# Kernel optimization log

Hardware: AMD Instinct MI355X
Metric: run time of the kernel (lower is better)

## Reference

```python
import jax, jax.numpy as jnp
import numpy as np

N, E, S = 50000, 800000, 3          # nodes, edges, message-passing steps
ND, ED, GD = 7, 4, 2                # raw node/edge/global feature dims
H, L = 64, 64                       # hidden and latent sizes


def _mlp3(x, W0, b0, W1, b1, W2, b2):
    # MLP([H, H, L]) with gelu between layers, none after last (dropout off).
    x = jax.nn.gelu(x @ W0 + b0)
    x = jax.nn.gelu(x @ W1 + b1)
    return x @ W2 + b2


def _ln(x, scale, bias, eps=1e-6):
    mu = jnp.mean(x, axis=-1, keepdims=True)
    xc = x - mu
    var = jnp.mean(xc * xc, axis=-1, keepdims=True)
    return xc * jax.lax.rsqrt(var + eps) * scale + bias


def setup_inputs() -> dict:
    key = jax.random.key(0)
    ks = iter(jax.random.split(key, 40))

    def W(i, o, stacked=False):
        shape = (S, i, o) if stacked else (i, o)
        return (jax.random.normal(next(ks), shape, jnp.float32) / np.sqrt(i)).astype(jnp.float32)

    inp = {
        "nodes": jax.random.normal(next(ks), (N, ND), jnp.float32),
        "edges": jax.random.normal(next(ks), (E, ED), jnp.float32),
        "glob": jax.random.normal(next(ks), (1, GD), jnp.float32),
        # node embedder MLP [H,H,L]
        "emb_n_W0": W(ND, H), "emb_n_b0": jnp.zeros((H,), jnp.float32),
        "emb_n_W1": W(H, H), "emb_n_b1": jnp.zeros((H,), jnp.float32),
        "emb_n_W2": W(H, L), "emb_n_b2": jnp.zeros((L,), jnp.float32),
        # edge embedder MLP
        "emb_e_W0": W(ED, H), "emb_e_b0": jnp.zeros((H,), jnp.float32),
        "emb_e_W1": W(H, H), "emb_e_b1": jnp.zeros((H,), jnp.float32),
        "emb_e_W2": W(H, L), "emb_e_b2": jnp.zeros((L,), jnp.float32),
        # per-step edge update MLP: in = edges(L)+senders(L)+receivers(L)+glob(GD)
        "edge_W0": W(3 * L + GD, H, True), "edge_b0": jnp.zeros((S, H), jnp.float32),
        "edge_W1": W(H, H, True), "edge_b1": jnp.zeros((S, H), jnp.float32),
        "edge_W2": W(H, L, True), "edge_b2": jnp.zeros((S, L), jnp.float32),
        # per-step node update MLP: in = nodes(L)+received(L)+glob(GD)
        "node_W0": W(2 * L + GD, H, True), "node_b0": jnp.zeros((S, H), jnp.float32),
        "node_W1": W(H, H, True), "node_b1": jnp.zeros((S, H), jnp.float32),
        "node_W2": W(H, L, True), "node_b2": jnp.zeros((S, L), jnp.float32),
        # per-step LayerNorms for nodes and edges
        "ln_n_scale": jnp.ones((S, L), jnp.float32), "ln_n_bias": jnp.zeros((S, L), jnp.float32),
        "ln_e_scale": jnp.ones((S, L), jnp.float32), "ln_e_bias": jnp.zeros((S, L), jnp.float32),
        # decoder MLP [H,H,3]
        "dec_W0": W(L, H), "dec_b0": jnp.zeros((H,), jnp.float32),
        "dec_W1": W(H, H), "dec_b1": jnp.zeros((H,), jnp.float32),
        "dec_W2": W(H, 3), "dec_b2": jnp.zeros((3,), jnp.float32),
        "senders": jax.random.randint(next(ks), (E,), 0, N),
        "receivers": jax.random.randint(next(ks), (E,), 0, N),
    }
    return inp


def reference(nodes, edges, glob,
              emb_n_W0, emb_n_b0, emb_n_W1, emb_n_b1, emb_n_W2, emb_n_b2,
              emb_e_W0, emb_e_b0, emb_e_W1, emb_e_b1, emb_e_W2, emb_e_b2,
              edge_W0, edge_b0, edge_W1, edge_b1, edge_W2, edge_b2,
              node_W0, node_b0, node_W1, node_b1, node_W2, node_b2,
              ln_n_scale, ln_n_bias, ln_e_scale, ln_e_bias,
              dec_W0, dec_b0, dec_W1, dec_b1, dec_W2, dec_b2,
              senders, receivers):
    # GraphMapFeatures embedder
    n = _mlp3(nodes, emb_n_W0, emb_n_b0, emb_n_W1, emb_n_b1, emb_n_W2, emb_n_b2)  # [N, L]
    e = _mlp3(edges, emb_e_W0, emb_e_b0, emb_e_W1, emb_e_b1, emb_e_W2, emb_e_b2)  # [E, L]
    n_nodes, n_edges = n.shape[0], e.shape[0]
    ge = jnp.broadcast_to(glob, (n_edges, glob.shape[1]))  # globals per edge (single graph)
    gn = jnp.broadcast_to(glob, (n_nodes, glob.shape[1]))  # globals per node
    steps = edge_W0.shape[0]
    for s in range(steps):
        # edge update: gather sender/receiver node feats, concat, MLP
        e_in = jnp.concatenate([e, n[senders], n[receivers], ge], axis=1)  # [E, 3L+GD]
        new_e = _mlp3(e_in, edge_W0[s], edge_b0[s], edge_W1[s], edge_b1[s], edge_W2[s], edge_b2[s])
        # scatter-aggregate to receivers (jraph default: segment_sum)
        recv = jax.ops.segment_sum(new_e, receivers, num_segments=n_nodes)  # [N, L]
        n_in = jnp.concatenate([n, recv, gn], axis=1)  # [N, 2L+GD]
        new_n = _mlp3(n_in, node_W0[s], node_b0[s], node_W1[s], node_b1[s], node_W2[s], node_b2[s])
        # residual skip connections then per-step LayerNorm
        n = _ln(n + new_n, ln_n_scale[s], ln_n_bias[s])
        e = _ln(e + new_e, ln_e_scale[s], ln_e_bias[s])
    # decoder on nodes -> [N, 3]
    return _mlp3(n, dec_W0, dec_b0, dec_W1, dec_b1, dec_W2, dec_b2)
```

## Files before the change

### kernel.cpp

```cpp
#include <hip/hip_runtime.h>

#define N_NODES 50000
#define N_EDGES 800000
#define NSTEPS 3
#define NBLK_SCAN 196

typedef __attribute__((ext_vector_type(8))) short bf16x8;
typedef __attribute__((ext_vector_type(4))) float f32x4;


__device__ __forceinline__ float ldf(const void* p, long i, int bf) {
    if (bf) {
        unsigned int u = ((const unsigned short*)p)[i];
        u <<= 16;
        return __uint_as_float(u);
    }
    return ((const float*)p)[i];
}

__device__ __forceinline__ unsigned short f2bf(float f) {
    return (unsigned short)((__float_as_uint(f) + 0x8000u) >> 16);
}

__device__ __forceinline__ float bf2f(unsigned short u) {
    return __uint_as_float(((unsigned int)u) << 16);
}

__device__ __forceinline__ float gelu_f(float x) {
    float x2 = x * x;
    float m = x * fmaf(-0.10294325f, x2, -2.30220847f);
    float e = __builtin_amdgcn_exp2f(m);
    return x * __builtin_amdgcn_rcpf(1.0f + e);
}

__device__ __forceinline__ void zero4(f32x4 a[4]) {
#pragma unroll
    for (int t = 0; t < 4; t++) a[t] = (f32x4){0.f, 0.f, 0.f, 0.f};
}

__device__ __forceinline__ void mfma_chunk(f32x4 acc[4], bf16x8 a, const unsigned short* bb) {
    acc[0] = __builtin_amdgcn_mfma_f32_16x16x32_bf16(a, *(const bf16x8*)(bb + 0), acc[0], 0, 0, 0);
    acc[1] = __builtin_amdgcn_mfma_f32_16x16x32_bf16(a, *(const bf16x8*)(bb + 512), acc[1], 0, 0, 0);
    acc[2] = __builtin_amdgcn_mfma_f32_16x16x32_bf16(a, *(const bf16x8*)(bb + 1024), acc[2], 0, 0, 0);
    acc[3] = __builtin_amdgcn_mfma_f32_16x16x32_bf16(a, *(const bf16x8*)(bb + 1536), acc[3], 0, 0, 0);
}

__global__ void detect_kernel(const void* probe, int* flag) {
    if (threadIdx.x == 0 && blockIdx.x == 0) {
        unsigned int w = *(const unsigned int*)probe;
        *flag = (w == 0x3F803F80u) ? 1 : 0;
    }
}

__global__ void hist_kernel(const int* __restrict__ receivers, int* __restrict__ counts) {
    int i = blockIdx.x * 256 + threadIdx.x;
    if (i < N_EDGES) atomicAdd(&counts[receivers[i]], 1);
}

__global__ void scan_partial(const int* __restrict__ counts, int* __restrict__ base,
                             int* __restrict__ blockSums) {
    __shared__ int sm[256];
    int b = blockIdx.x, t = threadIdx.x, i = b * 256 + t;
    int v = (i < N_NODES) ? counts[i] : 0;
    sm[t] = v;
    __syncthreads();
    for (int off = 1; off < 256; off <<= 1) {
        int x = (t >= off) ? sm[t - off] : 0;
        __syncthreads();
        sm[t] += x;
        __syncthreads();
    }
    if (i < N_NODES) base[i] = sm[t] - v;
    if (t == 255) blockSums[b] = sm[255];
}

__global__ void scan_tops(int* __restrict__ blockSums, int* __restrict__ tops) {
    __shared__ int sm[256];
    int t = threadIdx.x;
    int v = (t < NBLK_SCAN) ? blockSums[t] : 0;
    sm[t] = v;
    __syncthreads();
    for (int off = 1; off < 256; off <<= 1) {
        int x = (t >= off) ? sm[t - off] : 0;
        __syncthreads();
        sm[t] += x;
        __syncthreads();
    }
    if (t < NBLK_SCAN) tops[t] = sm[t] - v;
}

__global__ void scan_add(int* __restrict__ base, const int* __restrict__ tops,
                         int* __restrict__ cursor) {
    int b = blockIdx.x, i = b * 256 + threadIdx.x;
    if (i < N_NODES) {
        int v = base[i] + tops[b];
        base[i] = v;
        cursor[i] = v;
    }
}

__global__ void scatter_kernel(const int* __restrict__ senders,
                               const int* __restrict__ receivers, int* __restrict__ cursor,
                               int* __restrict__ ss, int* __restrict__ rsrt,
                               int* __restrict__ perm) {
    int i = blockIdx.x * 256 + threadIdx.x;
    if (i < N_EDGES) {
        int r = receivers[i];
        int pos = atomicAdd(&cursor[r], 1);
        ss[pos] = senders[i];
        rsrt[pos] = r;
        perm[pos] = i;
    }
}

struct PrepPtrs {
    const void* W[14];
    const void* eb0;
    const void* nb0;
    const void* glob;
};

#define PREP_WTOTAL 139264
__global__ void prep_all(PrepPtrs p, unsigned short* WbBase, float* b0eff_e, float* b0eff_n,
                         const int* __restrict__ flagp) {
    const int totals[14] = {36864, 12288, 12288, 24576, 12288, 12288, 2048,
                            4096,  4096,  2048,  4096,  4096,  4096,  4096};
    const int ksrc[14] = {192, 64, 64, 128, 64, 64, 7, 64, 64, 4, 64, 64, 64, 64};
    const int sstride[14] = {12416, 4096, 4096, 8320, 4096, 4096, 448,
                             4096,  4096, 256,  4096, 4096, 4096, 4096};
    const int nch[14] = {6, 2, 2, 4, 2, 2, 1, 2, 2, 1, 2, 2, 2, 2};

    const int bf = *flagp;
    int i = blockIdx.x * 256 + threadIdx.x;
    if (i < PREP_WTOTAL) {
        int e = 0, base = 0;
        while (i >= base + totals[e]) { base += totals[e]; e++; }
        int il = i - base;
        int j = il & 7, lane = (il >> 3) & 63, t = (il >> 9) & 3;
        int c = (il >> 11) % nch[e], s = il / (2048 * nch[e]);
        int k = c * 32 + (lane >> 4) * 8 + j;
        int col = t * 16 + (lane & 15);
        WbBase[i] = (k < ksrc[e]) ? f2bf(ldf(p.W[e], (long)s * sstride[e] + (long)k * 64 + col, bf))
                                  : (unsigned short)0;
    } else if (i < PREP_WTOTAL + 384) {
        int i2 = i - PREP_WTOTAL;
        float g0 = ldf(p.glob, 0, bf), g1 = ldf(p.glob, 1, bf);
        if (i2 < 192) {
            int s = i2 >> 6, col = i2 & 63;
            b0eff_e[i2] = ldf(p.eb0, i2, bf) + g0 * ldf(p.W[0], (long)s * 12416 + 192 * 64 + col, bf)
                                             + g1 * ldf(p.W[0], (long)s * 12416 + 193 * 64 + col, bf);
        } else {
            int il = i2 - 192;
            int s = il >> 6, col = il & 63;
            b0eff_n[il] = ldf(p.nb0, il, bf) + g0 * ldf(p.W[3], (long)s * 8320 + 128 * 64 + col, bf)
                                             + g1 * ldf(p.W[3], (long)s * 8320 + 129 * 64 + col, bf);
        }
    }
}

template <int DIN, int OUT_BF>
__global__ __launch_bounds__(256) void embed_mfma(
    const void* __restrict__ xin, const unsigned short* __restrict__ Wb0, const void* b0,
    const unsigned short* __restrict__ Wb1, const void* b1,
    const unsigned short* __restrict__ Wb2, const void* b2, void* __restrict__ outp,
    unsigned short* __restrict__ out_bf, const int* __restrict__ perm, int R,
    const int* __restrict__ flagp) {
    __shared__ __align__(16) unsigned short Xs[64 * 40];
    __shared__ __align__(16) unsigned short hbuf[64 * 72];
    const int bf = *flagp;
    const int tid = threadIdx.x;
    const long rb = (long)blockIdx.x * 64;
    const int lane = tid & 63, w = tid >> 6, q = lane >> 4, l15 = lane & 15;
    const int arow = 16 * w + l15, aoff = q * 8;
    unsigned short* hw = hbuf + w * 16 * 72;

    {
        int r = tid >> 2, seg = tid & 3;
        long idx = rb + r;
        long src = (perm != nullptr && idx < R) ? (long)perm[idx] : idx;
        unsigned short u[8];
#pragma unroll
        for (int j = 0; j < 8; j++) {
            int col = seg * 8 + j;
            u[j] = (col < DIN && idx < R) ? f2bf(ldf(xin, src * DIN + col, bf)) : (unsigned short)0;
        }
        *(uint4*)&Xs[r * 40 + seg * 8] = *(uint4*)u;
    }

    f32x4 acc[4];
    zero4(acc);
    {
        bf16x8 a = *(const bf16x8*)&Xs[arow * 40 + aoff];
        mfma_chunk(acc, a, Wb0 + lane * 8);
#pragma unroll
        for (int t = 0; t < 4; t++) {
            int col = t * 16 + l15;
            float b = ldf(b0, col, bf);
#pragma unroll
            for (int reg = 0; reg < 4; reg++)
                hw[(q * 4 + reg) * 72 + col] = f2bf(gelu_f(acc[t][reg] + b));
        }
    }
    zero4(acc);
    {
#pragma unroll
        for (int c = 0; c < 2; c++) {
            bf16x8 a = *(const bf16x8*)&hw[l15 * 72 + c * 32 + aoff];
            mfma_chunk(acc, a, Wb1 + c * 2048 + lane * 8);
        }
#pragma unroll
        for (int t = 0; t < 4; t++) {
            int col = t * 16 + l15;
            float b = ldf(b1, col, bf);
#pragma unroll
            for (int reg = 0; reg < 4; reg++)
                hw[(q * 4 + reg) * 72 + col] = f2bf(gelu_f(acc[t][reg] + b));
        }
    }
    zero4(acc);
    {
#pragma unroll
        for (int c = 0; c < 2; c++) {
            bf16x8 a = *(const bf16x8*)&hw[l15 * 72 + c * 32 + aoff];
            mfma_chunk(acc, a, Wb2 + c * 2048 + lane * 8);
        }
    }
    if (OUT_BF) {
#pragma unroll
        for (int t = 0; t < 4; t++) {
            int col = t * 16 + l15;
            float b = ldf(b2, col, bf);
#pragma unroll
            for (int reg = 0; reg < 4; reg++)
                hw[(q * 4 + reg) * 72 + col] = f2bf(acc[t][reg] + b);
        }
#pragma unroll
        for (int p = 0; p < 2; p++) {
            int r = 16 * w + p * 8 + (lane >> 3), o = lane & 7;
            long idx = rb + r;
            if (idx < R)
                *(uint4*)&((unsigned short*)outp)[idx * 64 + o * 8] =
                    *(const uint4*)&hbuf[r * 72 + o * 8];
        }
    } else {
#pragma unroll
        for (int t = 0; t < 4; t++) {
            int col = t * 16 + l15;
            float b = ldf(b2, col, bf);
#pragma unroll
            for (int reg = 0; reg < 4; reg++) {
                long idx = rb + 16 * w + q * 4 + reg;
                if (idx < R) {
                    float v = acc[t][reg] + b;
                    ((float*)outp)[idx * 64 + col] = v;
                    out_bf[idx * 64 + col] = f2bf(v);
                }
            }
        }
    }
}

#define EST 72
#define NST 68
template <int S0, int LAST>
__global__ __launch_bounds__(256) void edge_step(
    unsigned short* __restrict__ e_lat, const unsigned short* __restrict__ n_bf,
    const int* __restrict__ ss, const int* __restrict__ rsrt, const int* __restrict__ perm,
    const void* __restrict__ xe_raw, const unsigned short* __restrict__ We0, const void* eb0_,
    const unsigned short* __restrict__ We1, const void* eb1_,
    const unsigned short* __restrict__ We2, const void* eb2_,
    const unsigned short* __restrict__ Wb0, const unsigned short* __restrict__ Wb1,
    const unsigned short* __restrict__ Wb2, const float* __restrict__ b0eff, const void* b1,
    const void* b2, const void* lnsc, const void* lnbi, float* __restrict__ recvbuf, int s,
    const int* __restrict__ flagp) {
    __shared__ __align__(16) unsigned short Ee[64 * EST];
    __shared__ __align__(16) unsigned short NsNr[128 * NST];
    __shared__ int rcvs[64];
    float* newe = (float*)NsNr;

    const int bf = *flagp;
    const int tid = threadIdx.x;
    const long rb = (long)blockIdx.x * 64;
    const int lane = tid & 63, w = tid >> 6, q = lane >> 4, l15 = lane & 15;
    const int arow = 16 * w + l15, aoff = q * 8;
    unsigned short* hw = Ee + w * 16 * EST;

#pragma unroll
    for (int p = 0; p < 2; p++) {
        int r = 16 * w + p * 8 + (lane >> 3), o = lane & 7;
        long node = ss[rb + r];
        *(uint4*)&NsNr[r * NST + o * 8] = ((const uint4*)(n_bf + node * 64))[o];
    }
#pragma unroll
    for (int p = 0; p < 2; p++) {
        int r = 16 * w + p * 8 + (lane >> 3), o = lane & 7;
        long node = rsrt[rb + r];
        *(uint4*)&NsNr[(64 + r) * NST + o * 8] = ((const uint4*)(n_bf + node * 64))[o];
    }
    if (lane < 16) rcvs[16 * w + lane] = rsrt[rb + 16 * w + lane];

    float ein[4][4];
    f32x4 acc[4];

    if (S0) {
        zero4(acc);
        {
            bf16x8 a = (bf16x8){0, 0, 0, 0, 0, 0, 0, 0};
            if (q == 0) {
                long src = perm[rb + arow];
                unsigned short u[8] = {0, 0, 0, 0, 0, 0, 0, 0};
#pragma unroll
                for (int j = 0; j < 4; j++) u[j] = f2bf(ldf(xe_raw, src * 4 + j, bf));
                a = *(const bf16x8*)u;
            }
            mfma_chunk(acc, a, We0 + lane * 8);
#pragma unroll
            for (int t = 0; t < 4; t++) {
                int col = t * 16 + l15;
                float b = ldf(eb0_, col, bf);
#pragma unroll
                for (int reg = 0; reg < 4; reg++)
                    hw[(q * 4 + reg) * EST + col] = f2bf(gelu_f(acc[t][reg] + b));
            }
        }
        zero4(acc);
        {
#pragma unroll
            for (int c = 0; c < 2; c++) {
                bf16x8 a = *(const bf16x8*)&hw[l15 * EST + c * 32 + aoff];
                mfma_chunk(acc, a, We1 + c * 2048 + lane * 8);
            }
#pragma unroll
            for (int t = 0; t < 4; t++) {
                int col = t * 16 + l15;
                float b = ldf(eb1_, col, bf);
#pragma unroll
                for (int reg = 0; reg < 4; reg++)
                    hw[(q * 4 + reg) * EST + col] = f2bf(gelu_f(acc[t][reg] + b));
            }
        }
        zero4(acc);
        {
#pragma unroll
            for (int c = 0; c < 2; c++) {
                bf16x8 a = *(const bf16x8*)&hw[l15 * EST + c * 32 + aoff];
                mfma_chunk(acc, a, We2 + c * 2048 + lane * 8);
            }
#pragma unroll
            for (int t = 0; t < 4; t++) {
                int col = t * 16 + l15;
                float b = ldf(eb2_, col, bf);
#pragma unroll
                for (int reg = 0; reg < 4; reg++) {
                    ein[reg][t] = acc[t][reg] + b;
                    Ee[(16 * w + q * 4 + reg) * EST + col] = f2bf(ein[reg][t]);
                }
            }
        }
    } else {
#pragma unroll
        for (int p = 0; p < 2; p++) {
            int r = 16 * w + p * 8 + (lane >> 3), o = lane & 7;
            *(uint4*)&Ee[r * EST + o * 8] = ((const uint4*)(e_lat + (rb + r) * 64))[o];
        }
        if (!LAST) {
#pragma unroll
            for (int reg = 0; reg < 4; reg++)
#pragma unroll
                for (int t = 0; t < 4; t++)
                    ein[reg][t] = bf2f(Ee[(16 * w + q * 4 + reg) * EST + t * 16 + l15]);
        }
    }

    zero4(acc);
    {
        const unsigned short* B = Wb0 + (long)s * 6 * 2048 + lane * 8;
#pragma unroll
        for (int c = 0; c < 2; c++) {
            bf16x8 a = *(const bf16x8*)&Ee[arow * EST + c * 32 + aoff];
            mfma_chunk(acc, a, B + c * 2048);
        }
#pragma unroll
        for (int c = 0; c < 2; c++) {
            bf16x8 a = *(const bf16x8*)&NsNr[arow * NST + c * 32 + aoff];
            mfma_chunk(acc, a, B + (2 + c) * 2048);
        }
#pragma unroll
        for (int c = 0; c < 2; c++) {
            bf16x8 a = *(const bf16x8*)&NsNr[(64 + arow) * NST + c * 32 + aoff];
            mfma_chunk(acc, a, B + (4 + c) * 2048);
        }
#pragma unroll
        for (int t = 0; t < 4; t++) {
            const int col = t * 16 + l15;
            const float b = b0eff[s * 64 + col];
#pragma unroll
            for (int reg = 0; reg < 4; reg++)
                hw[(q * 4 + reg) * EST + col] = f2bf(gelu_f(acc[t][reg] + b));
        }
    }
    zero4(acc);
    {
        const unsigned short* B = Wb1 + (long)s * 2 * 2048 + lane * 8;
#pragma unroll
        for (int c = 0; c < 2; c++) {
            bf16x8 a = *(const bf16x8*)&hw[l15 * EST + c * 32 + aoff];
            mfma_chunk(acc, a, B + c * 2048);
        }
#pragma unroll
        for (int t = 0; t < 4; t++) {
            const int col = t * 16 + l15;
            const float b = ldf(b1, (long)s * 64 + col, bf);
#pragma unroll
            for (int reg = 0; reg < 4; reg++)
                hw[(q * 4 + reg) * EST + col] = f2bf(gelu_f(acc[t][reg] + b));
        }
    }
    zero4(acc);
    {
        const unsigned short* B = Wb2 + (long)s * 2 * 2048 + lane * 8;
#pragma unroll
        for (int c = 0; c < 2; c++) {
            bf16x8 a = *(const bf16x8*)&hw[l15 * EST + c * 32 + aoff];
            mfma_chunk(acc, a, B + c * 2048);
        }
    }
    __syncthreads();

    float fin[4][4];
#pragma unroll
    for (int t = 0; t < 4; t++) {
        const float b = ldf(b2, (long)s * 64 + t * 16 + l15, bf);
#pragma unroll
        for (int reg = 0; reg < 4; reg++) fin[reg][t] = acc[t][reg] + b;
    }
    float lsc[4], lbi[4];
    if (!LAST) {
#pragma unroll
        for (int t = 0; t < 4; t++) {
            lsc[t] = ldf(lnsc, (long)s * 64 + t * 16 + l15, bf);
            lbi[t] = ldf(lnbi, (long)s * 64 + t * 16 + l15, bf);
        }
    }
#pragma unroll
    for (int reg = 0; reg < 4; reg++) {
        const int lr = q * 4 + reg;
#pragma unroll
        for (int t = 0; t < 4; t++) newe[w * 1056 + lr * 66 + t * 16 + l15] = fin[reg][t];
        if (!LAST) {
            float u[4], ssum = 0.f;
#pragma unroll
            for (int t = 0; t < 4; t++) {
                u[t] = ein[reg][t] + fin[reg][t];
                ssum += u[t];
            }
#pragma unroll
            for (int m = 1; m < 16; m <<= 1) ssum += __shfl_xor(ssum, m, 64);
            const float mu = ssum * (1.0f / 64.0f);
            float d[4], vv = 0.f;
#pragma unroll
            for (int t = 0; t < 4; t++) { d[t] = u[t] - mu; vv += d[t] * d[t]; }
#pragma unroll
            for (int m = 1; m < 16; m <<= 1) vv += __shfl_xor(vv, m, 64);
            const float rs = rsqrtf(vv * (1.0f / 64.0f) + 1e-6f);
#pragma unroll
            for (int t = 0; t < 4; t++)
                Ee[(16 * w + lr) * EST + t * 16 + l15] = f2bf(d[t] * rs * lsc[t] + lbi[t]);
        }
    }

    if (!LAST) {
#pragma unroll
        for (int p = 0; p < 2; p++) {
            int r = 16 * w + p * 8 + (lane >> 3), o = lane & 7;
            *(uint4*)&e_lat[(rb + r) * 64 + o * 8] = *(const uint4*)&Ee[r * EST + o * 8];
        }
    }
    {
        const int col = tid & 63, g = tid >> 6;
        float a = 0.f;
#pragma unroll
        for (int rr = 0; rr < 16; rr++) {
            const int r = 16 * g + rr;
            a += newe[g * 1056 + rr * 66 + col];
            if (rr == 15 || rcvs[r + 1] != rcvs[r]) {
                atomicAdd(&recvbuf[(long)rcvs[r] * 64 + col], a);
                a = 0.f;
            }
        }
    }
}

#define NXS 136
template <int FINAL>
__global__ __launch_bounds__(256) void node_update_mfma(
    float* __restrict__ n_lat, unsigned short* __restrict__ n_bf, float* __restrict__ recvbuf,
    const unsigned short* __restrict__ Wb0, const float* __restrict__ b0eff,
    const unsigned short* __restrict__ Wb1, const void* b1,
    const unsigned short* __restrict__ Wb2, const void* b2, const void* lnsc,
    const void* lnbi, const unsigned short* __restrict__ WbD0, const void* db0,
    const unsigned short* __restrict__ WbD1, const void* db1, const void* dW2,
    const void* db2, void* __restrict__ outp, int s, const int* __restrict__ flagp) {
    __shared__ __align__(16) unsigned short Xs[64 * NXS];
    __shared__ __align__(16) unsigned short hbuf[64 * 72];
    const int bf = *flagp;
    const int tid = threadIdx.x;
    const long rb = (long)blockIdx.x * 64;
    const int lane = tid & 63, w = tid >> 6, q = lane >> 4, l15 = lane & 15;
    const int arow = 16 * w + l15, aoff = q * 8;
    unsigned short* hw = hbuf + w * 16 * 72;

#pragma unroll
    for (int p = 0; p < 2; p++) {
        int r = 16 * w + p * 8 + (lane >> 3), o = lane & 7;
        long idx = rb + r;
        uint4 v = {0u, 0u, 0u, 0u};
        if (idx < N_NODES) v = ((const uint4*)(n_bf + idx * 64))[o];
        *(uint4*)&Xs[r * NXS + o * 8] = v;
    }
#pragma unroll
    for (int p = 0; p < 2; p++) {
        int r = 16 * w + p * 8 + (lane >> 3), o = lane & 7;
        long idx = rb + r;
        unsigned short u[8] = {0, 0, 0, 0, 0, 0, 0, 0};
        if (idx < N_NODES) {
            const float* src = recvbuf + idx * 64 + o * 8;
            float4 x0 = *(const float4*)src, x1 = *(const float4*)(src + 4);
            u[0] = f2bf(x0.x); u[1] = f2bf(x0.y); u[2] = f2bf(x0.z); u[3] = f2bf(x0.w);
            u[4] = f2bf(x1.x); u[5] = f2bf(x1.y); u[6] = f2bf(x1.z); u[7] = f2bf(x1.w);
        }
        *(uint4*)&Xs[r * NXS + 64 + o * 8] = *(uint4*)u;
    }

    f32x4 acc[4];
    zero4(acc);
    {
        const unsigned short* B = Wb0 + (long)s * 4 * 2048 + lane * 8;
#pragma unroll
        for (int c = 0; c < 4; c++) {
            bf16x8 a = *(const bf16x8*)&Xs[arow * NXS + c * 32 + aoff];
            mfma_chunk(acc, a, B + c * 2048);
        }
#pragma unroll
        for (int t = 0; t < 4; t++) {
            const int col = t * 16 + l15;
            const float b = b0eff[s * 64 + col];
#pragma unroll
            for (int reg = 0; reg < 4; reg++)
                hw[(q * 4 + reg) * 72 + col] = f2bf(gelu_f(acc[t][reg] + b));
        }
    }
    zero4(acc);
    {
        const unsigned short* B = Wb1 + (long)s * 2 * 2048 + lane * 8;
#pragma unroll
        for (int c = 0; c < 2; c++) {
            bf16x8 a = *(const bf16x8*)&hw[l15 * 72 + c * 32 + aoff];
            mfma_chunk(acc, a, B + c * 2048);
        }
#pragma unroll
        for (int t = 0; t < 4; t++) {
            const int col = t * 16 + l15;
            const float b = ldf(b1, (long)s * 64 + col, bf);
#pragma unroll
            for (int reg = 0; reg < 4; reg++)
                hw[(q * 4 + reg) * 72 + col] = f2bf(gelu_f(acc[t][reg] + b));
        }
    }
    zero4(acc);
    {
        const unsigned short* B = Wb2 + (long)s * 2 * 2048 + lane * 8;
#pragma unroll
        for (int c = 0; c < 2; c++) {
            bf16x8 a = *(const bf16x8*)&hw[l15 * 72 + c * 32 + aoff];
            mfma_chunk(acc, a, B + c * 2048);
        }
    }
    float b2v[4], lsc[4], lbi[4];
#pragma unroll
    for (int t = 0; t < 4; t++) {
        b2v[t] = ldf(b2, (long)s * 64 + t * 16 + l15, bf);
        lsc[t] = ldf(lnsc, (long)s * 64 + t * 16 + l15, bf);
        lbi[t] = ldf(lnbi, (long)s * 64 + t * 16 + l15, bf);
    }
#pragma unroll
    for (int reg = 0; reg < 4; reg++) {
        const int rowl = 16 * w + q * 4 + reg;
        const long idx = rb + rowl;
        const bool valid = idx < N_NODES;
        float u[4], ssum = 0.f;
#pragma unroll
        for (int t = 0; t < 4; t++) {
            const int col = t * 16 + l15;
            float xn = valid ? n_lat[idx * 64 + col] : 0.f;
            u[t] = xn + acc[t][reg] + b2v[t];
            ssum += u[t];
        }
#pragma unroll
        for (int m = 1; m < 16; m <<= 1) ssum += __shfl_xor(ssum, m, 64);
        const float mu = ssum * (1.0f / 64.0f);
        float d[4], vv = 0.f;
#pragma unroll
        for (int t = 0; t < 4; t++) { d[t] = u[t] - mu; vv += d[t] * d[t]; }
#pragma unroll
        for (int m = 1; m < 16; m <<= 1) vv += __shfl_xor(vv, m, 64);
        const float rs = rsqrtf(vv * (1.0f / 64.0f) + 1e-6f);
        if (FINAL) {
#pragma unroll
            for (int t = 0; t < 4; t++) {
                const int col = t * 16 + l15;
                hw[(q * 4 + reg) * 72 + col] = f2bf(d[t] * rs * lsc[t] + lbi[t]);
            }
        } else if (valid) {
#pragma unroll
            for (int t = 0; t < 4; t++) {
                const int col = t * 16 + l15;
                float v = d[t] * rs * lsc[t] + lbi[t];
                n_lat[idx * 64 + col] = v;
                n_bf[idx * 64 + col] = f2bf(v);
                recvbuf[idx * 64 + col] = 0.f;
            }
        }
    }
    if (FINAL) {
        zero4(acc);
        {
#pragma unroll
            for (int c = 0; c < 2; c++) {
                bf16x8 a = *(const bf16x8*)&hw[l15 * 72 + c * 32 + aoff];
                mfma_chunk(acc, a, WbD0 + c * 2048 + lane * 8);
            }
#pragma unroll
            for (int t = 0; t < 4; t++) {
                const int col = t * 16 + l15;
                const float b = ldf(db0, col, bf);
#pragma unroll
                for (int reg = 0; reg < 4; reg++)
                    hw[(q * 4 + reg) * 72 + col] = f2bf(gelu_f(acc[t][reg] + b));
            }
        }
        zero4(acc);
        {
#pragma unroll
            for (int c = 0; c < 2; c++) {
                bf16x8 a = *(const bf16x8*)&hw[l15 * 72 + c * 32 + aoff];
                mfma_chunk(acc, a, WbD1 + c * 2048 + lane * 8);
            }
#pragma unroll
            for (int t = 0; t < 4; t++) {
                const int col = t * 16 + l15;
                const float b = ldf(db1, col, bf);
#pragma unroll
                for (int reg = 0; reg < 4; reg++)
                    hw[(q * 4 + reg) * 72 + col] = f2bf(gelu_f(acc[t][reg] + b));
            }
        }
        const int col = tid & 63;
        const int r0 = w * 16;
        if (col < 3) {
            float a[16];
            const float b = ldf(db2, col, bf);
#pragma unroll
            for (int i = 0; i < 16; i++) a[i] = b;
            for (int k = 0; k < 64; k++) {
                float wv = ldf(dW2, (long)k * 3 + col, bf);
#pragma unroll
                for (int i = 0; i < 16; i++) a[i] = fmaf(bf2f(hw[i * 72 + k]), wv, a[i]);
            }
            for (int i = 0; i < 16; i++) {
                const long idx = rb + r0 + i;
                if (idx < N_NODES) {
                    if (bf)
                        ((unsigned short*)outp)[idx * 3 + col] = f2bf(a[i]);
                    else
                        ((float*)outp)[idx * 3 + col] = a[i];
                }
            }
        }
    }
}

extern "C" void kernel_launch(void* const* d_in, const int* in_sizes, int n_in, void* d_out,
                              int out_size, void* d_ws, size_t ws_size, hipStream_t stream) {
    const void* nodes = d_in[0];
    const void* edges = d_in[1];
    const void* glob = d_in[2];
    const void *enW0 = d_in[3], *enb0 = d_in[4], *enW1 = d_in[5], *enb1 = d_in[6],
               *enW2 = d_in[7], *enb2 = d_in[8];
    const void *eeW0 = d_in[9], *eeb0 = d_in[10], *eeW1 = d_in[11], *eeb1 = d_in[12],
               *eeW2 = d_in[13], *eeb2 = d_in[14];
    const void *eW0 = d_in[15], *eb0 = d_in[16], *eW1 = d_in[17], *eb1 = d_in[18],
               *eW2 = d_in[19], *eb2 = d_in[20];
    const void *nW0 = d_in[21], *nb0 = d_in[22], *nW1 = d_in[23], *nb1 = d_in[24],
               *nW2 = d_in[25], *nb2 = d_in[26];
    const void *lnns = d_in[27], *lnnb = d_in[28], *lnes = d_in[29], *lneb = d_in[30];
    const void *dW0 = d_in[31], *db0 = d_in[32], *dW1 = d_in[33], *db1 = d_in[34],
               *dW2 = d_in[35], *db2 = d_in[36];
    const int* senders = (const int*)d_in[37];
    const int* receivers = (const int*)d_in[38];

    float* n_lat = (float*)d_ws;
    float* recvb = n_lat + 3200000;
    float* b0eff_e = recvb + 3200000;
    float* b0eff_n = b0eff_e + 192;
    int* flag = (int*)(b0eff_n + 192);
    unsigned short* e_lat = (unsigned short*)(b0eff_n + 256);
    unsigned short* n_bf = e_lat + 51200000;
    unsigned short* WbBase = n_bf + 3200000;
    unsigned short* WbE0 = WbBase;
    unsigned short* WbE1 = WbBase + 36864;
    unsigned short* WbE2 = WbBase + 49152;
    unsigned short* WbN0 = WbBase + 61440;
    unsigned short* WbN1 = WbBase + 86016;
    unsigned short* WbN2 = WbBase + 98304;
    unsigned short* WbNE0 = WbBase + 110592;
    unsigned short* WbNE1 = WbBase + 112640;
    unsigned short* WbNE2 = WbBase + 116736;
    unsigned short* WbEE0 = WbBase + 120832;
    unsigned short* WbEE1 = WbBase + 122880;
    unsigned short* WbEE2 = WbBase + 126976;
    unsigned short* WbD0 = WbBase + 131072;
    unsigned short* WbD1 = WbBase + 135168;
    int* counts = (int*)(WbBase + 139264 + 64);
    int* sbase = counts + N_NODES;
    int* cursor = sbase + N_NODES;
    int* blockSums = cursor + N_NODES;
    int* tops = blockSums + 256;
    int* ss = tops + 256;
    int* rsrt = ss + N_EDGES;
    int* perm = rsrt + N_EDGES;

    detect_kernel<<<1, 64, 0, stream>>>(lnns, flag);

    PrepPtrs pp;
    pp.W[0] = eW0;  pp.W[1] = eW1;  pp.W[2] = eW2;
    pp.W[3] = nW0;  pp.W[4] = nW1;  pp.W[5] = nW2;
    pp.W[6] = enW0; pp.W[7] = enW1; pp.W[8] = enW2;
    pp.W[9] = eeW0; pp.W[10] = eeW1; pp.W[11] = eeW2;
    pp.W[12] = dW0; pp.W[13] = dW1;
    pp.eb0 = eb0; pp.nb0 = nb0; pp.glob = glob;
    prep_all<<<(PREP_WTOTAL + 384 + 255) / 256, 256, 0, stream>>>(pp, WbBase, b0eff_e, b0eff_n,
                                                                  flag);
    hipMemsetAsync(recvb, 0, (size_t)N_NODES * 64 * sizeof(float), stream);
    hipMemsetAsync(counts, 0, (size_t)N_NODES * sizeof(int), stream);

    hist_kernel<<<(N_EDGES + 255) / 256, 256, 0, stream>>>(receivers, counts);
    scan_partial<<<NBLK_SCAN, 256, 0, stream>>>(counts, sbase, blockSums);
    scan_tops<<<1, 256, 0, stream>>>(blockSums, tops);
    scan_add<<<NBLK_SCAN, 256, 0, stream>>>(sbase, tops, cursor);
    scatter_kernel<<<(N_EDGES + 255) / 256, 256, 0, stream>>>(senders, receivers, cursor, ss,
                                                              rsrt, perm);

    embed_mfma<7, 0><<<(N_NODES + 63) / 64, 256, 0, stream>>>(
        nodes, WbNE0, enb0, WbNE1, enb1, WbNE2, enb2, n_lat, n_bf, (const int*)nullptr,
        N_NODES, flag);

    edge_step<1, 0><<<N_EDGES / 64, 256, 0, stream>>>(
        e_lat, n_bf, ss, rsrt, perm, edges, WbEE0, eeb0, WbEE1, eeb1, WbEE2, eeb2,
        WbE0, WbE1, WbE2, b0eff_e, eb1, eb2, lnes, lneb, recvb, 0, flag);
    node_update_mfma<0><<<(N_NODES + 63) / 64, 256, 0, stream>>>(
        n_lat, n_bf, recvb, WbN0, b0eff_n, WbN1, nb1, WbN2, nb2, lnns, lnnb,
        nullptr, nullptr, nullptr, nullptr, nullptr, nullptr, nullptr, 0, flag);

    edge_step<0, 0><<<N_EDGES / 64, 256, 0, stream>>>(
        e_lat, n_bf, ss, rsrt, perm, edges, WbEE0, eeb0, WbEE1, eeb1, WbEE2, eeb2,
        WbE0, WbE1, WbE2, b0eff_e, eb1, eb2, lnes, lneb, recvb, 1, flag);
    node_update_mfma<0><<<(N_NODES + 63) / 64, 256, 0, stream>>>(
        n_lat, n_bf, recvb, WbN0, b0eff_n, WbN1, nb1, WbN2, nb2, lnns, lnnb,
        nullptr, nullptr, nullptr, nullptr, nullptr, nullptr, nullptr, 1, flag);

    edge_step<0, 1><<<N_EDGES / 64, 256, 0, stream>>>(
        e_lat, n_bf, ss, rsrt, perm, edges, WbEE0, eeb0, WbEE1, eeb1, WbEE2, eeb2,
        WbE0, WbE1, WbE2, b0eff_e, eb1, eb2, lnes, lneb, recvb, 2, flag);
    node_update_mfma<1><<<(N_NODES + 63) / 64, 256, 0, stream>>>(
        n_lat, n_bf, recvb, WbN0, b0eff_n, WbN1, nb1, WbN2, nb2, lnns, lnnb,
        WbD0, db0, WbD1, db1, dW2, db2, d_out, 2, flag);
}
```

Measured before the change: 751.2 us.

## Store hidden activations in permuted column order with packed bf16 LDS writes

Stores intermediate activations in shared memory with a permuted column order (col t*16+l15 placed at l15*4+t), so each lane writes its four columns as one 8-byte store. Conversion uses the packed v_cvt_pk_bf16_f32 instruction. The weight rows of every following layer, and the decoder's last scalar weights, are permuted in prep to match. This replaces many scalar 2-byte LDS stores and conversions with fewer wide ones. The risk is LDS bank conflicts from the new layout, and any weight whose rows are not permuted consistently will give wrong results.

Result: faster. 670.0 us (-10.8%).

```diff
diff --git a/kernel.cpp b/kernel.cpp
--- a/kernel.cpp
+++ b/kernel.cpp
@@ -24,6 +24,12 @@
 
 __device__ __forceinline__ float bf2f(unsigned short u) {
     return __uint_as_float(((unsigned int)u) << 16);
+}
+
+__device__ __forceinline__ unsigned int cvtpk(float a, float b) {
+    unsigned int r;
+    asm("v_cvt_pk_bf16_f32 %0, %1, %2" : "=v"(r) : "v"(a), "v"(b));
+    return r;
 }
 
 __device__ __forceinline__ float gelu_f(float x) {
@@ -129,6 +135,7 @@
     const int sstride[14] = {12416, 4096, 4096, 8320, 4096, 4096, 448,
                              4096,  4096, 256,  4096, 4096, 4096, 4096};
     const int nch[14] = {6, 2, 2, 4, 2, 2, 1, 2, 2, 1, 2, 2, 2, 2};
+    const int rowperm[14] = {0, 1, 1, 0, 1, 1, 0, 1, 1, 0, 1, 1, 1, 1};
 
     const int bf = *flagp;
     int i = blockIdx.x * 256 + threadIdx.x;
@@ -140,7 +147,9 @@
         int c = (il >> 11) % nch[e], s = il / (2048 * nch[e]);
         int k = c * 32 + (lane >> 4) * 8 + j;
         int col = t * 16 + (lane & 15);
-        WbBase[i] = (k < ksrc[e]) ? f2bf(ldf(p.W[e], (long)s * sstride[e] + (long)k * 64 + col, bf))
+        int ks = k;
+        if (rowperm[e] || (e == 0 && k < 64)) ks = ((k & 3) << 4) | (k >> 2);
+        WbBase[i] = (k < ksrc[e]) ? f2bf(ldf(p.W[e], (long)s * sstride[e] + (long)ks * 64 + col, bf))
                                   : (unsigned short)0;
     } else if (i < PREP_WTOTAL + 384) {
         int i2 = i - PREP_WTOTAL;
@@ -192,13 +201,15 @@
     {
         bf16x8 a = *(const bf16x8*)&Xs[arow * 40 + aoff];
         mfma_chunk(acc, a, Wb0 + lane * 8);
-#pragma unroll
-        for (int t = 0; t < 4; t++) {
-            int col = t * 16 + l15;
-            float b = ldf(b0, col, bf);
-#pragma unroll
-            for (int reg = 0; reg < 4; reg++)
-                hw[(q * 4 + reg) * 72 + col] = f2bf(gelu_f(acc[t][reg] + b));
+        float bb[4];
+#pragma unroll
+        for (int t = 0; t < 4; t++) bb[t] = ldf(b0, t * 16 + l15, bf);
+#pragma unroll
+        for (int reg = 0; reg < 4; reg++) {
+            uint2 v;
+            v.x = cvtpk(gelu_f(acc[0][reg] + bb[0]), gelu_f(acc[1][reg] + bb[1]));
+            v.y = cvtpk(gelu_f(acc[2][reg] + bb[2]), gelu_f(acc[3][reg] + bb[3]));
+            *(uint2*)&hw[(q * 4 + reg) * 72 + l15 * 4] = v;
         }
     }
     zero4(acc);
@@ -208,13 +219,15 @@
             bf16x8 a = *(const bf16x8*)&hw[l15 * 72 + c * 32 + aoff];
             mfma_chunk(acc, a, Wb1 + c * 2048 + lane * 8);
         }
-#pragma unroll
-        for (int t = 0; t < 4; t++) {
-            int col = t * 16 + l15;
-            float b = ldf(b1, col, bf);
-#pragma unroll
-            for (int reg = 0; reg < 4; reg++)
-                hw[(q * 4 + reg) * 72 + col] = f2bf(gelu_f(acc[t][reg] + b));
+        float bb[4];
+#pragma unroll
+        for (int t = 0; t < 4; t++) bb[t] = ldf(b1, t * 16 + l15, bf);
+#pragma unroll
+        for (int reg = 0; reg < 4; reg++) {
+            uint2 v;
+            v.x = cvtpk(gelu_f(acc[0][reg] + bb[0]), gelu_f(acc[1][reg] + bb[1]));
+            v.y = cvtpk(gelu_f(acc[2][reg] + bb[2]), gelu_f(acc[3][reg] + bb[3]));
+            *(uint2*)&hw[(q * 4 + reg) * 72 + l15 * 4] = v;
         }
     }
     zero4(acc);
@@ -314,13 +327,15 @@
                 a = *(const bf16x8*)u;
             }
             mfma_chunk(acc, a, We0 + lane * 8);
-#pragma unroll
-            for (int t = 0; t < 4; t++) {
-                int col = t * 16 + l15;
-                float b = ldf(eb0_, col, bf);
-#pragma unroll
-                for (int reg = 0; reg < 4; reg++)
-                    hw[(q * 4 + reg) * EST + col] = f2bf(gelu_f(acc[t][reg] + b));
+            float bb[4];
+#pragma unroll
+            for (int t = 0; t < 4; t++) bb[t] = ldf(eb0_, t * 16 + l15, bf);
+#pragma unroll
+            for (int reg = 0; reg < 4; reg++) {
+                uint2 v;
+                v.x = cvtpk(gelu_f(acc[0][reg] + bb[0]), gelu_f(acc[1][reg] + bb[1]));
+                v.y = cvtpk(gelu_f(acc[2][reg] + bb[2]), gelu_f(acc[3][reg] + bb[3]));
+                *(uint2*)&hw[(q * 4 + reg) * EST + l15 * 4] = v;
             }
         }
         zero4(acc);
@@ -330,13 +345,15 @@
                 bf16x8 a = *(const bf16x8*)&hw[l15 * EST + c * 32 + aoff];
                 mfma_chunk(acc, a, We1 + c * 2048 + lane * 8);
             }
-#pragma unroll
-            for (int t = 0; t < 4; t++) {
-                int col = t * 16 + l15;
-                float b = ldf(eb1_, col, bf);
-#pragma unroll
-                for (int reg = 0; reg < 4; reg++)
-                    hw[(q * 4 + reg) * EST + col] = f2bf(gelu_f(acc[t][reg] + b));
+            float bb[4];
+#pragma unroll
+            for (int t = 0; t < 4; t++) bb[t] = ldf(eb1_, t * 16 + l15, bf);
+#pragma unroll
+            for (int reg = 0; reg < 4; reg++) {
+                uint2 v;
+                v.x = cvtpk(gelu_f(acc[0][reg] + bb[0]), gelu_f(acc[1][reg] + bb[1]));
+                v.y = cvtpk(gelu_f(acc[2][reg] + bb[2]), gelu_f(acc[3][reg] + bb[3]));
+                *(uint2*)&hw[(q * 4 + reg) * EST + l15 * 4] = v;
             }
         }
         zero4(acc);
@@ -346,15 +363,18 @@
                 bf16x8 a = *(const bf16x8*)&hw[l15 * EST + c * 32 + aoff];
                 mfma_chunk(acc, a, We2 + c * 2048 + lane * 8);
             }
-#pragma unroll
-            for (int t = 0; t < 4; t++) {
-                int col = t * 16 + l15;
-                float b = ldf(eb2_, col, bf);
-#pragma unroll
-                for (int reg = 0; reg < 4; reg++) {
-                    ein[reg][t] = acc[t][reg] + b;
-                    Ee[(16 * w + q * 4 + reg) * EST + col] = f2bf(ein[reg][t]);
-                }
+            float bb[4];
+#pragma unroll
+            for (int t = 0; t < 4; t++) bb[t] = ldf(eb2_, t * 16 + l15, bf);
+#pragma unroll
+            for (int reg = 0; reg < 4; reg++) {
+                float e0 = acc[0][reg] + bb[0], e1 = acc[1][reg] + bb[1];
+                float e2 = acc[2][reg] + bb[2], e3 = acc[3][reg] + bb[3];
+                ein[reg][0] = e0; ein[reg][1] = e1; ein[reg][2] = e2; ein[reg][3] = e3;
+                uint2 v;
+                v.x = cvtpk(e0, e1);
+                v.y = cvtpk(e2, e3);
+                *(uint2*)&Ee[(16 * w + q * 4 + reg) * EST + l15 * 4] = v;
             }
         }
     } else {
@@ -365,10 +385,13 @@
         }
         if (!LAST) {
 #pragma unroll
-            for (int reg = 0; reg < 4; reg++)
-#pragma unroll
-                for (int t = 0; t < 4; t++)
-                    ein[reg][t] = bf2f(Ee[(16 * w + q * 4 + reg) * EST + t * 16 + l15]);
+            for (int reg = 0; reg < 4; reg++) {
+                uint2 pv = *(const uint2*)&Ee[(16 * w + q * 4 + reg) * EST + l15 * 4];
+                ein[reg][0] = __uint_as_float(pv.x << 16);
+                ein[reg][1] = __uint_as_float(pv.x & 0xffff0000u);
+                ein[reg][2] = __uint_as_float(pv.y << 16);
+                ein[reg][3] = __uint_as_float(pv.y & 0xffff0000u);
+            }
         }
     }
 
@@ -390,13 +413,15 @@
             bf16x8 a = *(const bf16x8*)&NsNr[(64 + arow) * NST + c * 32 + aoff];
             mfma_chunk(acc, a, B + (4 + c) * 2048);
         }
-#pragma unroll
-        for (int t = 0; t < 4; t++) {
-            const int col = t * 16 + l15;
-            const float b = b0eff[s * 64 + col];
-#pragma unroll
-            for (int reg = 0; reg < 4; reg++)
-                hw[(q * 4 + reg) * EST + col] = f2bf(gelu_f(acc[t][reg] + b));
+        float bb[4];
+#pragma unroll
+        for (int t = 0; t < 4; t++) bb[t] = b0eff[s * 64 + t * 16 + l15];
+#pragma unroll
+        for (int reg = 0; reg < 4; reg++) {
+            uint2 v;
+            v.x = cvtpk(gelu_f(acc[0][reg] + bb[0]), gelu_f(acc[1][reg] + bb[1]));
+            v.y = cvtpk(gelu_f(acc[2][reg] + bb[2]), gelu_f(acc[3][reg] + bb[3]));
+            *(uint2*)&hw[(q * 4 + reg) * EST + l15 * 4] = v;
         }
     }
     zero4(acc);
@@ -407,13 +432,15 @@
             bf16x8 a = *(const bf16x8*)&hw[l15 * EST + c * 32 + aoff];
             mfma_chunk(acc, a, B + c * 2048);
         }
-#pragma unroll
-        for (int t = 0; t < 4; t++) {
-            const int col = t * 16 + l15;
-            const float b = ldf(b1, (long)s * 64 + col, bf);
-#pragma unroll
-            for (int reg = 0; reg < 4; reg++)
-                hw[(q * 4 + reg) * EST + col] = f2bf(gelu_f(acc[t][reg] + b));
+        float bb[4];
+#pragma unroll
+        for (int t = 0; t < 4; t++) bb[t] = ldf(b1, (long)s * 64 + t * 16 + l15, bf);
+#pragma unroll
+        for (int reg = 0; reg < 4; reg++) {
+            uint2 v;
+            v.x = cvtpk(gelu_f(acc[0][reg] + bb[0]), gelu_f(acc[1][reg] + bb[1]));
+            v.y = cvtpk(gelu_f(acc[2][reg] + bb[2]), gelu_f(acc[3][reg] + bb[3]));
+            *(uint2*)&hw[(q * 4 + reg) * EST + l15 * 4] = v;
         }
     }
     zero4(acc);
@@ -463,9 +490,10 @@
 #pragma unroll
             for (int m = 1; m < 16; m <<= 1) vv += __shfl_xor(vv, m, 64);
             const float rs = rsqrtf(vv * (1.0f / 64.0f) + 1e-6f);
-#pragma unroll
-            for (int t = 0; t < 4; t++)
-                Ee[(16 * w + lr) * EST + t * 16 + l15] = f2bf(d[t] * rs * lsc[t] + lbi[t]);
+            uint2 v;
+            v.x = cvtpk(d[0] * rs * lsc[0] + lbi[0], d[1] * rs * lsc[1] + lbi[1]);
+            v.y = cvtpk(d[2] * rs * lsc[2] + lbi[2], d[3] * rs * lsc[3] + lbi[3]);
+            *(uint2*)&Ee[(16 * w + lr) * EST + l15 * 4] = v;
         }
     }
 
@@ -522,14 +550,16 @@
     for (int p = 0; p < 2; p++) {
         int r = 16 * w + p * 8 + (lane >> 3), o = lane & 7;
         long idx = rb + r;
-        unsigned short u[8] = {0, 0, 0, 0, 0, 0, 0, 0};
+        uint4 v = {0u, 0u, 0u, 0u};
         if (idx < N_NODES) {
             const float* src = recvbuf + idx * 64 + o * 8;
             float4 x0 = *(const float4*)src, x1 = *(const float4*)(src + 4);
-            u[0] = f2bf(x0.x); u[1] = f2bf(x0.y); u[2] = f2bf(x0.z); u[3] = f2bf(x0.w);
-            u[4] = f2bf(x1.x); u[5] = f2bf(x1.y); u[6] = f2bf(x1.z); u[7] = f2bf(x1.w);
-        }
-        *(uint4*)&Xs[r * NXS + 64 + o * 8] = *(uint4*)u;
+            v.x = cvtpk(x0.x, x0.y);
+            v.y = cvtpk(x0.z, x0.w);
+            v.z = cvtpk(x1.x, x1.y);
+            v.w = cvtpk(x1.z, x1.w);
+        }
+        *(uint4*)&Xs[r * NXS + 64 + o * 8] = v;
     }
 
     f32x4 acc[4];
@@ -541,13 +571,15 @@
             bf16x8 a = *(const bf16x8*)&Xs[arow * NXS + c * 32 + aoff];
             mfma_chunk(acc, a, B + c * 2048);
         }
-#pragma unroll
-        for (int t = 0; t < 4; t++) {
-            const int col = t * 16 + l15;
-            const float b = b0eff[s * 64 + col];
-#pragma unroll
-            for (int reg = 0; reg < 4; reg++)
-                hw[(q * 4 + reg) * 72 + col] = f2bf(gelu_f(acc[t][reg] + b));
+        float bb[4];
+#pragma unroll
+        for (int t = 0; t < 4; t++) bb[t] = b0eff[s * 64 + t * 16 + l15];
+#pragma unroll
+        for (int reg = 0; reg < 4; reg++) {
+            uint2 v;
+            v.x = cvtpk(gelu_f(acc[0][reg] + bb[0]), gelu_f(acc[1][reg] + bb[1]));
+            v.y = cvtpk(gelu_f(acc[2][reg] + bb[2]), gelu_f(acc[3][reg] + bb[3]));
+            *(uint2*)&hw[(q * 4 + reg) * 72 + l15 * 4] = v;
         }
     }
     zero4(acc);
@@ -558,13 +590,15 @@
             bf16x8 a = *(const bf16x8*)&hw[l15 * 72 + c * 32 + aoff];
             mfma_chunk(acc, a, B + c * 2048);
         }
-#pragma unroll
-        for (int t = 0; t < 4; t++) {
-            const int col = t * 16 + l15;
-            const float b = ldf(b1, (long)s * 64 + col, bf);
-#pragma unroll
-            for (int reg = 0; reg < 4; reg++)
-                hw[(q * 4 + reg) * 72 + col] = f2bf(gelu_f(acc[t][reg] + b));
+        float bb[4];
+#pragma unroll
+        for (int t = 0; t < 4; t++) bb[t] = ldf(b1, (long)s * 64 + t * 16 + l15, bf);
+#pragma unroll
+        for (int reg = 0; reg < 4; reg++) {
+            uint2 v;
+            v.x = cvtpk(gelu_f(acc[0][reg] + bb[0]), gelu_f(acc[1][reg] + bb[1]));
+            v.y = cvtpk(gelu_f(acc[2][reg] + bb[2]), gelu_f(acc[3][reg] + bb[3]));
+            *(uint2*)&hw[(q * 4 + reg) * 72 + l15 * 4] = v;
         }
     }
     zero4(acc);
@@ -606,11 +640,10 @@
         for (int m = 1; m < 16; m <<= 1) vv += __shfl_xor(vv, m, 64);
         const float rs = rsqrtf(vv * (1.0f / 64.0f) + 1e-6f);
         if (FINAL) {
-#pragma unroll
-            for (int t = 0; t < 4; t++) {
-                const int col = t * 16 + l15;
-                hw[(q * 4 + reg) * 72 + col] = f2bf(d[t] * rs * lsc[t] + lbi[t]);
-            }
+            uint2 v;
+            v.x = cvtpk(d[0] * rs * lsc[0] + lbi[0], d[1] * rs * lsc[1] + lbi[1]);
+            v.y = cvtpk(d[2] * rs * lsc[2] + lbi[2], d[3] * rs * lsc[3] + lbi[3]);
+            *(uint2*)&hw[(q * 4 + reg) * 72 + l15 * 4] = v;
         } else if (valid) {
 #pragma unroll
             for (int t = 0; t < 4; t++) {
@@ -630,13 +663,15 @@
                 bf16x8 a = *(const bf16x8*)&hw[l15 * 72 + c * 32 + aoff];
                 mfma_chunk(acc, a, WbD0 + c * 2048 + lane * 8);
             }
-#pragma unroll
-            for (int t = 0; t < 4; t++) {
-                const int col = t * 16 + l15;
-                const float b = ldf(db0, col, bf);
-#pragma unroll
-                for (int reg = 0; reg < 4; reg++)
-                    hw[(q * 4 + reg) * 72 + col] = f2bf(gelu_f(acc[t][reg] + b));
+            float bb[4];
+#pragma unroll
+            for (int t = 0; t < 4; t++) bb[t] = ldf(db0, t * 16 + l15, bf);
+#pragma unroll
+            for (int reg = 0; reg < 4; reg++) {
+                uint2 v;
+                v.x = cvtpk(gelu_f(acc[0][reg] + bb[0]), gelu_f(acc[1][reg] + bb[1]));
+                v.y = cvtpk(gelu_f(acc[2][reg] + bb[2]), gelu_f(acc[3][reg] + bb[3]));
+                *(uint2*)&hw[(q * 4 + reg) * 72 + l15 * 4] = v;
             }
         }
         zero4(acc);
@@ -646,13 +681,15 @@
                 bf16x8 a = *(const bf16x8*)&hw[l15 * 72 + c * 32 + aoff];
                 mfma_chunk(acc, a, WbD1 + c * 2048 + lane * 8);
             }
-#pragma unroll
-            for (int t = 0; t < 4; t++) {
-                const int col = t * 16 + l15;
-                const float b = ldf(db1, col, bf);
-#pragma unroll
-                for (int reg = 0; reg < 4; reg++)
-                    hw[(q * 4 + reg) * 72 + col] = f2bf(gelu_f(acc[t][reg] + b));
+            float bb[4];
+#pragma unroll
+            for (int t = 0; t < 4; t++) bb[t] = ldf(db1, t * 16 + l15, bf);
+#pragma unroll
+            for (int reg = 0; reg < 4; reg++) {
+                uint2 v;
+                v.x = cvtpk(gelu_f(acc[0][reg] + bb[0]), gelu_f(acc[1][reg] + bb[1]));
+                v.y = cvtpk(gelu_f(acc[2][reg] + bb[2]), gelu_f(acc[3][reg] + bb[3]));
+                *(uint2*)&hw[(q * 4 + reg) * 72 + l15 * 4] = v;
             }
         }
         const int col = tid & 63;
@@ -663,7 +700,8 @@
 #pragma unroll
             for (int i = 0; i < 16; i++) a[i] = b;
             for (int k = 0; k < 64; k++) {
-                float wv = ldf(dW2, (long)k * 3 + col, bf);
+                const int ksrc2 = ((k & 3) << 4) | (k >> 2);
+                float wv = ldf(dW2, (long)ksrc2 * 3 + col, bf);
 #pragma unroll
                 for (int i = 0; i < 16; i++) a[i] = fmaf(bf2f(hw[i * 72 + k]), wv, a[i]);
             }
```
